# Optimization experiments

Hardware: AMD Instinct MI355X
Metric: run time of the kernel (lower is better)

## Reference

```python
import jax, jax.numpy as jnp
import numpy as np

N = 4096
NHID = 256
K1, K2, K3 = 3072, 2304, 1728


def _layernorm(x, g, b, eps=1e-5):
    m = jnp.mean(x, axis=-1, keepdims=True)
    v = jnp.mean((x - m) ** 2, axis=-1, keepdims=True)
    return (x - m) / jnp.sqrt(v + eps) * g + b


def _gcn(x, A, W, b):
    # PyG GCNConv: add self loops, symmetric norm D^-1/2 (A+I) D^-1/2,
    # messages flow row(source) -> col(target): out[j] = sum_i Anorm[i,j] (xW)[i] + b
    n = A.shape[0]
    A_sl = A + jnp.eye(n, dtype=A.dtype)
    deg = A_sl.sum(0)  # in-degree over col index incl. self loop
    dinv = jnp.where(deg > 0, deg ** -0.5, 0.0)
    An = A_sl * dinv[:, None] * dinv[None, :]
    return An.T @ (x @ W) + b


def _sagpool(x, A, Wp, bp, k):
    score = jnp.tanh(_gcn(x, A, Wp, bp)[:, 0])  # [n]
    vals, perm = jax.lax.top_k(score, k)
    x_new = x[perm] * vals[:, None]
    A_new = A[perm][:, perm]  # induced subgraph of directed edges
    return x_new, A_new


def _readout(x):
    # cat([global_max_pool, global_mean_pool]) for a single graph -> [1, 2*nhid]
    return jnp.concatenate([x.max(0), x.mean(0)])[None, :]


def setup_inputs() -> dict:
    key = jax.random.key(0)
    ks = jax.random.split(key, 10)
    s = 0.05
    return {
        'feature': jax.random.normal(ks[0], (N, 500), jnp.float32),
        'img_info': jax.random.normal(ks[1], (N, 6), jnp.float32),
        'Wp': jax.random.normal(ks[2], (6, 12), jnp.float32) * s,
        'bp': jnp.zeros((12,), jnp.float32),
        'ln_f_g': jnp.ones((500,), jnp.float32),
        'ln_f_b': jnp.zeros((500,), jnp.float32),
        'ln_p_g': jnp.ones((12,), jnp.float32),
        'ln_p_b': jnp.zeros((12,), jnp.float32),
        'W1': jax.random.normal(ks[3], (512, NHID), jnp.float32) * s,
        'b1': jnp.zeros((NHID,), jnp.float32),
        'Wpool1': jax.random.normal(ks[4], (NHID, 1), jnp.float32) * s,
        'bpool1': jnp.zeros((1,), jnp.float32),
        'W2': jax.random.normal(ks[5], (NHID, NHID), jnp.float32) * s,
        'b2': jnp.zeros((NHID,), jnp.float32),
        'Wpool2': jax.random.normal(ks[6], (NHID, 1), jnp.float32) * s,
        'bpool2': jnp.zeros((1,), jnp.float32),
        'W3': jax.random.normal(ks[7], (NHID, NHID), jnp.float32) * s,
        'b3': jnp.zeros((NHID,), jnp.float32),
        'Wpool3': jax.random.normal(ks[8], (NHID, 1), jnp.float32) * s,
        'bpool3': jnp.zeros((1,), jnp.float32),
    }


def reference(feature, img_info, Wp, bp, ln_f_g, ln_f_b, ln_p_g, ln_p_b,
              W1, b1, Wpool1, bpool1, W2, b2, Wpool2, bpool2,
              W3, b3, Wpool3, bpool3):
    # pos embedding + self-attention over nodes
    pos = img_info @ Wp + bp                                  # [N,12]
    att = jax.nn.softmax(pos @ pos.T / jnp.sqrt(12.0), axis=1)  # [N,N]
    pos = att @ pos

    f = _layernorm(feature, ln_f_g, ln_f_b)
    p = _layernorm(pos, ln_p_g, ln_p_b)
    x0 = jnp.concatenate([f, p], axis=1)                      # [N,512]

    # edge construction: upper-triangular directed edges where sqdist < 0.5*max sqdist
    sq = jnp.sum(x0 * x0, axis=1)
    d2 = sq[:, None] - 2.0 * (x0 @ x0.T) + sq[None, :]        # [N,N]
    t = 0.5 * d2.max()
    n = x0.shape[0]
    iu = jnp.triu(jnp.ones((n, n), bool), 1)
    A = jnp.where((d2 < t) & iu, 1.0, 0.0).astype(x0.dtype)

    x = jax.nn.relu(_gcn(x0, A, W1, b1))
    x, A = _sagpool(x, A, Wpool1, bpool1, K1)
    x1 = _readout(x)

    x = jax.nn.relu(_gcn(x, A, W2, b2))
    x, A = _sagpool(x, A, Wpool2, bpool2, K2)
    x2 = _readout(x)

    x = jax.nn.relu(_gcn(x, A, W3, b3))
    x, A = _sagpool(x, A, Wpool3, bpool3, K3)
    x3 = _readout(x)

    return x1 + x2 + x3  # [1, 512]
```

## Files before the change

kernel.cpp:

```cpp
#include <hip/hip_runtime.h>
#include <math.h>

#define NN 4096
#define RB 128

typedef __attribute__((ext_vector_type(8))) short bf16x8;
typedef __attribute__((ext_vector_type(4))) float f32x4;

__device__ __forceinline__ unsigned encf(float f) {
  unsigned u = __float_as_uint(f);
  return (u & 0x80000000u) ? ~u : (u | 0x80000000u);
}
__device__ __forceinline__ float decf(unsigned u) {
  return __uint_as_float((u & 0x80000000u) ? (u ^ 0x80000000u) : ~u);
}
__device__ __forceinline__ unsigned short f2bf(float f) {
  unsigned u = __float_as_uint(f);
  return (unsigned short)((u + 0x7fffu + ((u >> 16) & 1u)) >> 16);
}

__global__ void k_pos(const float* img, const float* Wp, const float* bp, float* pos,
                      unsigned* dmax) {
  if (blockIdx.x == 0 && threadIdx.x == 0) *dmax = 0u;
  int t = blockIdx.x * 256 + threadIdx.x;
  if (t >= NN * 12) return;
  int i = t / 12, d = t % 12;
  float s = bp[d];
#pragma unroll
  for (int k = 0; k < 6; ++k) s += img[i * 6 + k] * Wp[k * 12 + d];
  pos[t] = s;
}

__global__ __launch_bounds__(256) void k_attn3(const float* pos, float* out) {
  __shared__ float sp[12][256];
  int t = threadIdx.x, lane = t & 63, w = t >> 6;
  int ib = blockIdx.x * 8 + w * 2;
  float pi[2][12];
#pragma unroll
  for (int r = 0; r < 2; ++r)
#pragma unroll
    for (int d = 0; d < 12; ++d) pi[r][d] = pos[(ib + r) * 12 + d] * 0.28867513459481287f;
  float sl[2] = {0.f, 0.f};
  float acc[2][12] = {};
  const float4* p4 = (const float4*)pos;
  for (int kt = 0; kt < NN; kt += 256) {
    __syncthreads();
    int j = kt + t;
    float4 a = p4[j * 3 + 0], b = p4[j * 3 + 1], c = p4[j * 3 + 2];
    sp[0][t] = a.x; sp[1][t] = a.y; sp[2][t] = a.z; sp[3][t] = a.w;
    sp[4][t] = b.x; sp[5][t] = b.y; sp[6][t] = b.z; sp[7][t] = b.w;
    sp[8][t] = c.x; sp[9][t] = c.y; sp[10][t] = c.z; sp[11][t] = c.w;
    __syncthreads();
#pragma unroll
    for (int q = 0; q < 4; ++q) {
      int jj = q * 64 + lane;
      float pj[12];
#pragma unroll
      for (int d = 0; d < 12; ++d) pj[d] = sp[d][jj];
#pragma unroll
      for (int r = 0; r < 2; ++r) {
        float s = 0.f;
#pragma unroll
        for (int d = 0; d < 12; ++d) s = fmaf(pi[r][d], pj[d], s);
        float e = __expf(s);
        sl[r] += e;
#pragma unroll
        for (int d = 0; d < 12; ++d) acc[r][d] = fmaf(e, pj[d], acc[r][d]);
      }
    }
  }
#pragma unroll
  for (int r = 0; r < 2; ++r) {
    float s = sl[r];
#pragma unroll
    for (int o = 32; o > 0; o >>= 1) s += __shfl_xor(s, o);
    float ad[12];
#pragma unroll
    for (int d = 0; d < 12; ++d) {
      ad[d] = acc[r][d];
#pragma unroll
      for (int o = 32; o > 0; o >>= 1) ad[d] += __shfl_xor(ad[d], o);
    }
    if (lane == 0) {
      float inv = 1.f / s;
#pragma unroll
      for (int d = 0; d < 12; ++d) out[(ib + r) * 12 + d] = ad[d] * inv;
    }
  }
}

__global__ __launch_bounds__(256) void k_lnx(const float* f, const float* g, const float* b,
                                             const float* p, const float* pg, const float* pb,
                                             float* x0, unsigned short* x0h, float* sqv,
                                             int* degA) {
  __shared__ float row[512];
  __shared__ float wrA[4], wrB[4], wrC[4];
  int i = blockIdx.x, t = threadIdx.x, lane = t & 63, w = t >> 6;
  if (t == 0) degA[i] = 0;
  float v1 = f[i * 500 + t];
  float v2 = (t < 244) ? f[i * 500 + 256 + t] : 0.f;
  float part = v1 + v2;
#pragma unroll
  for (int o = 32; o > 0; o >>= 1) part += __shfl_xor(part, o);
  if (lane == 0) wrA[w] = part;
  __syncthreads();
  float m = (wrA[0] + wrA[1] + wrA[2] + wrA[3]) * (1.f / 500.f);
  float d1 = v1 - m, d2 = v2 - m;
  float pvv = d1 * d1 + ((t < 244) ? d2 * d2 : 0.f);
#pragma unroll
  for (int o = 32; o > 0; o >>= 1) pvv += __shfl_xor(pvv, o);
  if (lane == 0) wrB[w] = pvv;
  __syncthreads();
  float scale = 1.f / sqrtf((wrB[0] + wrB[1] + wrB[2] + wrB[3]) * (1.f / 500.f) + 1e-5f);
  row[t] = d1 * scale * g[t] + b[t];
  if (t < 244) row[256 + t] = d2 * scale * g[256 + t] + b[256 + t];
  if (t >= 244) {
    int tt = t - 244;
    float pv[12], pm = 0.f;
#pragma unroll
    for (int d = 0; d < 12; ++d) { pv[d] = p[i * 12 + d]; pm += pv[d]; }
    pm *= (1.f / 12.f);
    float pvar = 0.f;
#pragma unroll
    for (int d = 0; d < 12; ++d) { float dd = pv[d] - pm; pvar += dd * dd; }
    pvar *= (1.f / 12.f);
    float ps = 1.f / sqrtf(pvar + 1e-5f);
    row[500 + tt] = (pv[tt] - pm) * ps * pg[tt] + pb[tt];
  }
  __syncthreads();
  float a = row[t], c = row[256 + t];
  float sq = a * a + c * c;
#pragma unroll
  for (int o = 32; o > 0; o >>= 1) sq += __shfl_xor(sq, o);
  if (lane == 0) wrC[w] = sq;
  __syncthreads();
  if (t == 0) sqv[i] = wrC[0] + wrC[1] + wrC[2] + wrC[3];
  x0[(size_t)i * 512 + t] = a;
  x0[(size_t)i * 512 + 256 + t] = c;
  x0h[(size_t)i * 512 + t] = f2bf(a);
  x0h[(size_t)i * 512 + 256 + t] = f2bf(c);
}

#define BK 64
template <bool MASK>
__global__ __launch_bounds__(256) void k_d2m(const unsigned short* X, const float* sqv,
                                             unsigned* dmax, float* tileMin,
                                             unsigned char* ATm, int* deg) {
  __shared__ unsigned short As[2][128 * BK];
  __shared__ unsigned short Bs[2][128 * BK];
  __shared__ float wmax[4], wmin[4];
  const int NT = NN / 128;
  int bid0 = blockIdx.x;
  int bid = (bid0 & 7) * 66 + (bid0 >> 3);
  int ti = 0, rem = bid;
  while (rem >= NT - ti) { rem -= NT - ti; ++ti; }
  int tj = ti + rem;
  int t = threadIdx.x, lane = t & 63, w = t >> 6;
  int wr = w >> 1, wc = w & 1;
  const unsigned short* Abase = X + (size_t)ti * 128 * 512;
  const unsigned short* Bbase = X + (size_t)tj * 128 * 512;
  int lr = lane >> 3, lc = lane & 7;

  float thr = 0.f;
  if (MASK) {
    thr = 0.5f * decf(*dmax);
    uint4 z = make_uint4(0u, 0u, 0u, 0u);
    if (ti != tj) {
#pragma unroll
      for (int q0 = 0; q0 < 4; ++q0) {
        int q = t + q0 * 256; int r = q >> 3, c4 = q & 7;
        *(uint4*)(ATm + (size_t)(ti * 128 + r) * NN + tj * 128 + c4 * 16) = z;
      }
    }
    if (tileMin[blockIdx.x] >= thr) {
#pragma unroll
      for (int q0 = 0; q0 < 4; ++q0) {
        int q = t + q0 * 256; int r = q >> 3, c4 = q & 7;
        *(uint4*)(ATm + (size_t)(tj * 128 + r) * NN + ti * 128 + c4 * 16) = z;
      }
      return;
    }
  }

  auto stage = [&](int buf, int k0) {
#pragma unroll
    for (int i = 0; i < 4; ++i) {
      int q = w * 4 + i;
      int r = q * 8 + lr;
      int cs = lc ^ (r & 7);
      __builtin_amdgcn_global_load_lds(
          (const __attribute__((address_space(1))) unsigned int*)(Abase + (size_t)r * 512 + k0 + cs * 8),
          (__attribute__((address_space(3))) unsigned int*)(&As[buf][q * 512]), 16, 0, 0);
      __builtin_amdgcn_global_load_lds(
          (const __attribute__((address_space(1))) unsigned int*)(Bbase + (size_t)r * 512 + k0 + cs * 8),
          (__attribute__((address_space(3))) unsigned int*)(&Bs[buf][q * 512]), 16, 0, 0);
    }
  };

  stage(0, 0);

  f32x4 acc[4][4] = {};
  int rl = lane & 15, kg = lane >> 4;
  for (int step = 0; step < 8; ++step) {
    int cur = step & 1;
    if (step < 7) {
      stage(cur ^ 1, (step + 1) * BK);
      asm volatile("s_waitcnt vmcnt(8)" ::: "memory");
    } else {
      asm volatile("s_waitcnt vmcnt(0)" ::: "memory");
    }
    __builtin_amdgcn_sched_barrier(0);
    __builtin_amdgcn_s_barrier();
    __builtin_amdgcn_s_setprio(1);
#pragma unroll
    for (int ks = 0; ks < 2; ++ks) {
      bf16x8 af[4], bq[4];
#pragma unroll
      for (int f = 0; f < 4; ++f) {
        int rA = wr * 64 + f * 16 + rl;
        af[f] = *(const bf16x8*)(&As[cur][rA * BK + (((ks * 4 + kg) ^ (rA & 7)) << 3)]);
        int rB = wc * 64 + f * 16 + rl;
        bq[f] = *(const bf16x8*)(&Bs[cur][rB * BK + (((ks * 4 + kg) ^ (rB & 7)) << 3)]);
      }
#pragma unroll
      for (int a = 0; a < 4; ++a)
#pragma unroll
        for (int b = 0; b < 4; ++b)
          acc[a][b] = __builtin_amdgcn_mfma_f32_16x16x32_bf16(af[a], bq[b], acc[a][b], 0, 0, 0);
    }
    __builtin_amdgcn_s_setprio(0);
    __builtin_amdgcn_sched_barrier(0);
    __builtin_amdgcn_s_barrier();
  }
  int rbase = ti * 128 + wr * 64 + ((lane >> 4) << 2);
  int cbase = tj * 128 + wc * 64 + (lane & 15);
  if (!MASK) {
    float lm = -1e30f, lmin = 1e30f;
#pragma unroll
    for (int a = 0; a < 4; ++a) {
      float si[4];
#pragma unroll
      for (int r = 0; r < 4; ++r) si[r] = sqv[rbase + a * 16 + r];
#pragma unroll
      for (int b = 0; b < 4; ++b) {
        int gj = cbase + b * 16;
        float sj = sqv[gj];
#pragma unroll
        for (int r = 0; r < 4; ++r) {
          float d2v = si[r] - 2.f * acc[a][b][r] + sj;
          lm = fmaxf(lm, d2v);
          if (rbase + a * 16 + r < gj) lmin = fminf(lmin, d2v);
        }
      }
    }
#pragma unroll
    for (int o = 32; o > 0; o >>= 1) {
      lm = fmaxf(lm, __shfl_xor(lm, o));
      lmin = fminf(lmin, __shfl_xor(lmin, o));
    }
    if (lane == 0) { wmax[w] = lm; wmin[w] = lmin; }
    __syncthreads();
    if (t == 0) {
      atomicMax(dmax, encf(fmaxf(fmaxf(wmax[0], wmax[1]), fmaxf(wmax[2], wmax[3]))));
      tileMin[blockIdx.x] = fminf(fminf(wmin[0], wmin[1]), fminf(wmin[2], wmin[3]));
    }
  } else {
#pragma unroll
    for (int b = 0; b < 4; ++b) {
      int gj = cbase + b * 16;
      float sj = sqv[gj];
      int rowcnt = 0;
#pragma unroll
      for (int a = 0; a < 4; ++a) {
        int gi0 = rbase + a * 16;
        union { unsigned char c[4]; unsigned u; } m4;
#pragma unroll
        for (int r = 0; r < 4; ++r) {
          float d2v = sqv[gi0 + r] - 2.f * acc[a][b][r] + sj;
          unsigned char mv = (d2v < thr && (gi0 + r) < gj) ? 1 : 0;
          m4.c[r] = mv; rowcnt += mv;
        }
        *(unsigned*)(ATm + (size_t)gj * NN + gi0) = m4.u;
      }
      if (rowcnt) atomicAdd(&deg[gj], rowcnt);
    }
  }
}

__global__ __launch_bounds__(256) void k_gemm(const float* A, const float* B, const int* deg,
                                              float* C, int M, int N, int K) {
  __shared__ float Ast[16][34];
  __shared__ float Bs[16][64];
  int t = threadIdx.x, tx = t & 15, ty = t >> 4;
  int nbx = N >> 6;
  int total = gridDim.x;
  int bid0 = blockIdx.x;
  int bid = (bid0 & 7) * (total >> 3) + (bid0 >> 3);
  int m0 = (bid / nbx) * 32, n0 = (bid % nbx) * 64;
  int ar = t >> 3, ac = (t * 2) & 15;
  int br = t >> 4, bc = (t & 15) * 4;
  float2 ra = *(const float2*)(A + (size_t)(m0 + ar) * K + ac);
  float4 rb = *(const float4*)(B + (size_t)br * N + n0 + bc);
  float acc[2][4] = {};
  for (int k0 = 0; k0 < K; k0 += 16) {
    Ast[ac][ar] = ra.x; Ast[ac + 1][ar] = ra.y;
    *(float4*)(&Bs[br][bc]) = rb;
    __syncthreads();
    if (k0 + 16 < K) {
      ra = *(const float2*)(A + (size_t)(m0 + ar) * K + k0 + 16 + ac);
      rb = *(const float4*)(B + (size_t)(k0 + 16 + br) * N + n0 + bc);
    }
#pragma unroll
    for (int kk = 0; kk < 16; ++kk) {
      float2 av = *(const float2*)(&Ast[kk][ty * 2]);
      float4 bv = *(const float4*)(&Bs[kk][tx * 4]);
      acc[0][0] = fmaf(av.x, bv.x, acc[0][0]);
      acc[0][1] = fmaf(av.x, bv.y, acc[0][1]);
      acc[0][2] = fmaf(av.x, bv.z, acc[0][2]);
      acc[0][3] = fmaf(av.x, bv.w, acc[0][3]);
      acc[1][0] = fmaf(av.y, bv.x, acc[1][0]);
      acc[1][1] = fmaf(av.y, bv.y, acc[1][1]);
      acc[1][2] = fmaf(av.y, bv.z, acc[1][2]);
      acc[1][3] = fmaf(av.y, bv.w, acc[1][3]);
    }
    __syncthreads();
  }
#pragma unroll
  for (int a = 0; a < 2; ++a) {
    float dv = 1.f / sqrtf((float)(1 + deg[m0 + ty * 2 + a]));
#pragma unroll
    for (int b2 = 0; b2 < 4; ++b2)
      C[(size_t)(m0 + ty * 2 + a) * N + n0 + tx * 4 + b2] = acc[a][b2] * dv;
  }
}

__global__ __launch_bounds__(256) void k_agg(const float* y, const unsigned char* ATm,
                                             const int* deg, const float* bias,
                                             const float* Wpool, float* out, float* y2, int n) {
  __shared__ unsigned char mrow[256];
  __shared__ int s_any;
  __shared__ float wred[4];
  int j = blockIdx.x, t = threadIdx.x, lane = t & 63, w = t >> 6;
  int dg = deg[j];
  float dj = 1.f / sqrtf((float)(1 + dg));
  float acc = y[(size_t)j * 256 + t];
  if (dg != 0) {
    for (int i0 = 0; i0 < n; i0 += 256) {
      if (t == 0) s_any = 0;
      __syncthreads();
      unsigned char m = ATm[(size_t)j * n + i0 + t];
      mrow[t] = m;
      if (m) s_any = 1;
      __syncthreads();
      if (s_any) {
        for (int u = 0; u < 256; ++u)
          if (mrow[u]) acc += y[(size_t)(i0 + u) * 256 + t];
      }
      __syncthreads();
    }
  }
  float o = fmaxf(dj * acc + bias[t], 0.f);
  out[(size_t)j * 256 + t] = o;
  float rv = o * Wpool[t];
#pragma unroll
  for (int os = 32; os > 0; os >>= 1) rv += __shfl_xor(rv, os);
  if (lane == 0) wred[w] = rv;
  __syncthreads();
  if (t == 0) y2[j] = dj * (wred[0] + wred[1] + wred[2] + wred[3]);
}

__global__ __launch_bounds__(256) void k_scorek(const float* y2, const unsigned char* ATm,
                                                const int* deg, const float* bp,
                                                float* score, int n) {
  int w = threadIdx.x >> 6, lane = threadIdx.x & 63;
  int j = blockIdx.x * 4 + w;
  if (j >= n) return;
  int dg = deg[j];
  float dj = 1.f / sqrtf((float)(1 + dg));
  float s = 0.f;
  if (dg != 0) {
    const uint4* row = (const uint4*)(ATm + (size_t)j * n);
    for (int p = lane; p < n / 16; p += 64) {
      uint4 v = row[p];
      if (v.x | v.y | v.z | v.w) {
        int base = p * 16;
#pragma unroll
        for (int q = 0; q < 4; ++q) {
          unsigned u = (&v.x)[q];
#pragma unroll
          for (int b2 = 0; b2 < 4; ++b2)
            if ((u >> (8 * b2)) & 0xffu) s += y2[base + q * 4 + b2];
        }
      }
    }
    for (int sh = 32; sh > 0; sh >>= 1) s += __shfl_down(s, sh);
  }
  if (lane == 0) score[j] = tanhf(dj * (y2[j] + s) + bp[0]);
}

__global__ __launch_bounds__(1024) void k_topsel(const float* score, int n, int k,
                                                 int* perm, float* vals) {
  __shared__ unsigned keys[4096];
  __shared__ unsigned hist[256];
  __shared__ unsigned s_state[2];
  __shared__ unsigned woff[16];
  int t = threadIdx.x, lane = t & 63, w = t >> 6;
  for (int i = t; i < 4096; i += 1024) keys[i] = (i < n) ? encf(score[i]) : 0u;
  if (t == 0) { s_state[0] = 0u; s_state[1] = (unsigned)k; }
  __syncthreads();

  for (int pass = 0; pass < 4; ++pass) {
    int shift = 24 - pass * 8;
    if (t < 256) hist[t] = 0u;
    __syncthreads();
    unsigned prefix = s_state[0];
    unsigned need = s_state[1];
    unsigned pmask = pass ? (0xFFFFFFFFu << (shift + 8)) : 0u;
    for (int i = t; i < n; i += 1024) {
      unsigned kk = keys[i];
      if ((kk & pmask) == prefix) atomicAdd(&hist[(kk >> shift) & 255u], 1u);
    }
    __syncthreads();
    if (w == 0) {
      unsigned h[4], suf[4];
#pragma unroll
      for (int r = 0; r < 4; ++r) h[r] = hist[lane * 4 + r];
      suf[3] = h[3]; suf[2] = h[2] + suf[3]; suf[1] = h[1] + suf[2]; suf[0] = h[0] + suf[1];
      unsigned lsum = suf[0];
      unsigned s = lsum;
#pragma unroll
      for (int off = 1; off < 64; off <<= 1) {
        unsigned o = __shfl_down(s, off);
        if (lane + off < 64) s += o;
      }
      unsigned Hl = s - lsum;
      int cand = -1; unsigned cumAt = 0, histAt = 0;
#pragma unroll
      for (int r = 0; r < 4; ++r) {
        unsigned c = Hl + suf[r];
        if (c >= need) { cand = lane * 4 + r; cumAt = c; histAt = h[r]; }
      }
      int gmax = cand;
#pragma unroll
      for (int off = 32; off > 0; off >>= 1) {
        int o = __shfl_xor(gmax, off);
        gmax = o > gmax ? o : gmax;
      }
      if (cand == gmax && cand >= 0) {
        s_state[0] = prefix | ((unsigned)cand << shift);
        s_state[1] = need - (cumAt - histAt);
      }
    }
    __syncthreads();
  }
  unsigned cutoff = s_state[0];
  unsigned tcount = s_state[1];
  unsigned G = (unsigned)k - tcount;

  int i0 = t * 4;
  unsigned loc[4], cnt = 0;
#pragma unroll
  for (int r = 0; r < 4; ++r) {
    unsigned kk = keys[i0 + r];
    unsigned g = (kk > cutoff) ? 1u : 0u;
    unsigned e = (kk == cutoff) ? 1u : 0u;
    loc[r] = cnt;
    cnt += (g << 16) | e;
  }
  unsigned inc = cnt;
#pragma unroll
  for (int off = 1; off < 64; off <<= 1) {
    unsigned o = __shfl_up(inc, off);
    if (lane >= off) inc += o;
  }
  if (lane == 63) woff[w] = inc;
  __syncthreads();
  if (t == 0) {
    unsigned run = 0;
    for (int q = 0; q < 16; ++q) { unsigned v = woff[q]; woff[q] = run; run += v; }
  }
  __syncthreads();
  unsigned base = woff[w] + (inc - cnt);
#pragma unroll
  for (int r = 0; r < 4; ++r) {
    unsigned kk = keys[i0 + r];
    unsigned p = base + loc[r];
    if (kk > cutoff) {
      unsigned pos = p >> 16;
      perm[pos] = i0 + r; vals[pos] = decf(kk);
    } else if (kk == cutoff) {
      unsigned pe = p & 0xffffu;
      if (pe < tcount) { perm[G + pe] = i0 + r; vals[G + pe] = decf(kk); }
    }
  }
}

__global__ __launch_bounds__(256) void k_pool(const float* xg, const int* perm, const float* vals,
                                              float* xp, float* pmax, float* psum, int k,
                                              const unsigned char* ATold, const int* degCur,
                                              unsigned char* ATnew, int* degNext, int nold) {
  __shared__ int sperm[4096];
  __shared__ int redi[256];
  int b = blockIdx.x, t = threadIdx.x;
  if (b < RB) {
    float m = -1e30f, s = 0.f;
    for (int r = b; r < k; r += RB) {
      float v = xg[(size_t)perm[r] * 256 + t] * vals[r];
      xp[(size_t)r * 256 + t] = v;
      m = fmaxf(m, v); s += v;
    }
    pmax[b * 256 + t] = m; psum[b * 256 + t] = s;
    return;
  }
  int c = b - RB;
  for (int r = t; r < k; r += 256) sperm[r] = perm[r];
  __syncthreads();
  int src = sperm[c];
  unsigned char* orow = ATnew + (size_t)c * k;
  if (degCur[src] == 0) {
    uint4 z = make_uint4(0u, 0u, 0u, 0u);
    for (int r = t; r < k / 16; r += 256) ((uint4*)orow)[r] = z;
    if (t == 0) degNext[c] = 0;
    return;
  }
  const unsigned char* row = ATold + (size_t)src * nold;
  int cnt = 0;
  for (int r = t; r < k; r += 256) { unsigned char v = row[sperm[r]]; orow[r] = v; cnt += v; }
  redi[t] = cnt; __syncthreads();
  for (int s = 128; s > 0; s >>= 1) { if (t < s) redi[t] += redi[t + s]; __syncthreads(); }
  if (t == 0) degNext[c] = redi[0];
}

__global__ void k_rfin3(const float* pm0, const float* ps0, int k0,
                        const float* pm1, const float* ps1, int k1,
                        const float* pm2, const float* ps2, int k2, float* out) {
  int t = threadIdx.x;
  float m0 = -1e30f, s0 = 0.f, m1 = -1e30f, s1 = 0.f, m2 = -1e30f, s2 = 0.f;
  for (int q = 0; q < RB; ++q) {
    m0 = fmaxf(m0, pm0[q * 256 + t]); s0 += ps0[q * 256 + t];
    m1 = fmaxf(m1, pm1[q * 256 + t]); s1 += ps1[q * 256 + t];
    m2 = fmaxf(m2, pm2[q * 256 + t]); s2 += ps2[q * 256 + t];
  }
  out[t] = m0 + m1 + m2;
  out[256 + t] = s0 / (float)k0 + s1 / (float)k1 + s2 / (float)k2;
}

static void run_layer(hipStream_t stream, const float* x_in, int n, int inC,
                      const float* W, const float* b, const float* Wpool, const float* bpool,
                      int k, const unsigned char* ATcur, unsigned char* ATnext,
                      const int* degCur, int* degNext,
                      float* ybuf, float* xg, float* xp, float* y2,
                      float* score, int* perm, float* vals, float* pmax, float* psum) {
  k_gemm<<<(n / 32) * 4, 256, 0, stream>>>(x_in, W, degCur, ybuf, n, 256, inC);
  k_agg<<<n, 256, 0, stream>>>(ybuf, ATcur, degCur, b, Wpool, xg, y2, n);
  k_scorek<<<n / 4, 256, 0, stream>>>(y2, ATcur, degCur, bpool, score, n);
  k_topsel<<<1, 1024, 0, stream>>>(score, n, k, perm, vals);
  int grid = RB + (ATnext ? k : 0);
  k_pool<<<grid, 256, 0, stream>>>(xg, perm, vals, xp, pmax, psum, k,
                                   ATcur, degCur, ATnext, degNext, n);
}

extern "C" void kernel_launch(void* const* d_in, const int* in_sizes, int n_in,
                              void* d_out, int out_size, void* d_ws, size_t ws_size,
                              hipStream_t stream) {
  const float* feature = (const float*)d_in[0];
  const float* img     = (const float*)d_in[1];
  const float* Wp      = (const float*)d_in[2];
  const float* bp      = (const float*)d_in[3];
  const float* ln_f_g  = (const float*)d_in[4];
  const float* ln_f_b  = (const float*)d_in[5];
  const float* ln_p_g  = (const float*)d_in[6];
  const float* ln_p_b  = (const float*)d_in[7];
  const float* W1 = (const float*)d_in[8];   const float* b1 = (const float*)d_in[9];
  const float* Wpool1 = (const float*)d_in[10]; const float* bpool1 = (const float*)d_in[11];
  const float* W2 = (const float*)d_in[12];  const float* b2 = (const float*)d_in[13];
  const float* Wpool2 = (const float*)d_in[14]; const float* bpool2 = (const float*)d_in[15];
  const float* W3 = (const float*)d_in[16];  const float* b3 = (const float*)d_in[17];
  const float* Wpool3 = (const float*)d_in[18]; const float* bpool3 = (const float*)d_in[19];
  float* out = (float*)d_out;
  (void)in_sizes; (void)n_in; (void)out_size; (void)ws_size;

  char* w = (char*)d_ws;
  size_t off = 0;
  auto alloc = [&](size_t bytes) -> char* {
    off = (off + 255) & ~(size_t)255;
    char* p = w + off;
    off += bytes;
    return p;
  };
  float* pos0 = (float*)alloc((size_t)NN * 12 * 4);
  float* pos1 = (float*)alloc((size_t)NN * 12 * 4);
  float* x0   = (float*)alloc((size_t)NN * 512 * 4);
  unsigned short* x0h = (unsigned short*)alloc((size_t)NN * 512 * 2);
  float* sqv  = (float*)alloc((size_t)NN * 4);
  unsigned* dmax = (unsigned*)alloc(4);
  float* tileMin = (float*)alloc(528 * 4);
  int* degA = (int*)alloc((size_t)NN * 4);
  int* degB = (int*)alloc((size_t)NN * 4);
  float* ybuf = (float*)alloc((size_t)NN * 256 * 4);
  float* xg   = (float*)alloc((size_t)NN * 256 * 4);
  float* xp   = (float*)alloc((size_t)NN * 256 * 4);
  float* y2   = (float*)alloc((size_t)NN * 4);
  float* score= (float*)alloc((size_t)NN * 4);
  int*   perm = (int*)alloc((size_t)NN * 4);
  float* vals = (float*)alloc((size_t)NN * 4);
  float* pmax0 = (float*)alloc(RB * 256 * 4);
  float* psum0 = (float*)alloc(RB * 256 * 4);
  float* pmax1 = (float*)alloc(RB * 256 * 4);
  float* psum1 = (float*)alloc(RB * 256 * 4);
  float* pmax2 = (float*)alloc(RB * 256 * 4);
  float* psum2 = (float*)alloc(RB * 256 * 4);
  unsigned char* ATa = (unsigned char*)alloc((size_t)NN * NN);
  unsigned char* ATb = (unsigned char*)alloc((size_t)3072 * 3072);

  k_pos<<<(NN * 12 + 255) / 256, 256, 0, stream>>>(img, Wp, bp, pos0, dmax);
  k_attn3<<<NN / 8, 256, 0, stream>>>(pos0, pos1);
  k_lnx<<<NN, 256, 0, stream>>>(feature, ln_f_g, ln_f_b, pos1, ln_p_g, ln_p_b,
                                x0, x0h, sqv, degA);

  const int NT = NN / 128, TT = NT * (NT + 1) / 2;
  k_d2m<false><<<TT, 256, 0, stream>>>(x0h, sqv, dmax, tileMin, nullptr, nullptr);
  k_d2m<true><<<TT, 256, 0, stream>>>(x0h, sqv, dmax, tileMin, ATa, degA);

  run_layer(stream, x0, 4096, 512, W1, b1, Wpool1, bpool1, 3072, ATa, ATb, degA, degB,
            ybuf, xg, xp, y2, score, perm, vals, pmax0, psum0);
  run_layer(stream, xp, 3072, 256, W2, b2, Wpool2, bpool2, 2304, ATb, ATa, degB, degA,
            ybuf, xg, xp, y2, score, perm, vals, pmax1, psum1);
  run_layer(stream, xp, 2304, 256, W3, b3, Wpool3, bpool3, 1728, ATa, nullptr, degA, nullptr,
            ybuf, xg, xp, y2, score, perm, vals, pmax2, psum2);
  k_rfin3<<<1, 256, 0, stream>>>(pmax0, psum0, 3072, pmax1, psum1, 2304,
                                 pmax2, psum2, 1728, out);
}
```

Measured before the change: 217.4 us.

## Shrink GEMM tile, move isolated-node scores into agg, skip dead pool writes

The feature GEMM tile drops from 32 to 16 rows, which doubles the block count and makes each thread produce four outputs instead of eight, giving more parallelism for the small row counts. Nodes with zero degree now get their pool score computed in the aggregation kernel, so the score kernel returns early for them. The pool kernel skips zeroing adjacency rows of isolated nodes and only loads the permutation into shared memory when it is needed. The last layer skips writing the pooled features, since nothing reads them. Leaving those adjacency rows unzeroed relies on later kernels never reading rows whose degree is zero.

```diff
diff --git a/kernel.cpp b/kernel.cpp
--- a/kernel.cpp
+++ b/kernel.cpp
@@ -289,54 +289,48 @@
 
 __global__ __launch_bounds__(256) void k_gemm(const float* A, const float* B, const int* deg,
                                               float* C, int M, int N, int K) {
-  __shared__ float Ast[16][34];
+  __shared__ float Ast[16][17];
   __shared__ float Bs[16][64];
   int t = threadIdx.x, tx = t & 15, ty = t >> 4;
   int nbx = N >> 6;
   int total = gridDim.x;
   int bid0 = blockIdx.x;
   int bid = (bid0 & 7) * (total >> 3) + (bid0 >> 3);
-  int m0 = (bid / nbx) * 32, n0 = (bid % nbx) * 64;
-  int ar = t >> 3, ac = (t * 2) & 15;
+  int m0 = (bid / nbx) * 16, n0 = (bid % nbx) * 64;
+  int ar = t >> 4, ac = t & 15;
   int br = t >> 4, bc = (t & 15) * 4;
-  float2 ra = *(const float2*)(A + (size_t)(m0 + ar) * K + ac);
+  float ra = A[(size_t)(m0 + ar) * K + ac];
   float4 rb = *(const float4*)(B + (size_t)br * N + n0 + bc);
-  float acc[2][4] = {};
+  float acc[4] = {};
   for (int k0 = 0; k0 < K; k0 += 16) {
-    Ast[ac][ar] = ra.x; Ast[ac + 1][ar] = ra.y;
+    Ast[ac][ar] = ra;
     *(float4*)(&Bs[br][bc]) = rb;
     __syncthreads();
     if (k0 + 16 < K) {
-      ra = *(const float2*)(A + (size_t)(m0 + ar) * K + k0 + 16 + ac);
+      ra = A[(size_t)(m0 + ar) * K + k0 + 16 + ac];
       rb = *(const float4*)(B + (size_t)(k0 + 16 + br) * N + n0 + bc);
     }
 #pragma unroll
     for (int kk = 0; kk < 16; ++kk) {
-      float2 av = *(const float2*)(&Ast[kk][ty * 2]);
+      float av = Ast[kk][ty];
       float4 bv = *(const float4*)(&Bs[kk][tx * 4]);
-      acc[0][0] = fmaf(av.x, bv.x, acc[0][0]);
-      acc[0][1] = fmaf(av.x, bv.y, acc[0][1]);
-      acc[0][2] = fmaf(av.x, bv.z, acc[0][2]);
-      acc[0][3] = fmaf(av.x, bv.w, acc[0][3]);
-      acc[1][0] = fmaf(av.y, bv.x, acc[1][0]);
-      acc[1][1] = fmaf(av.y, bv.y, acc[1][1]);
-      acc[1][2] = fmaf(av.y, bv.z, acc[1][2]);
-      acc[1][3] = fmaf(av.y, bv.w, acc[1][3]);
-    }
-    __syncthreads();
-  }
-#pragma unroll
-  for (int a = 0; a < 2; ++a) {
-    float dv = 1.f / sqrtf((float)(1 + deg[m0 + ty * 2 + a]));
-#pragma unroll
-    for (int b2 = 0; b2 < 4; ++b2)
-      C[(size_t)(m0 + ty * 2 + a) * N + n0 + tx * 4 + b2] = acc[a][b2] * dv;
-  }
+      acc[0] = fmaf(av, bv.x, acc[0]);
+      acc[1] = fmaf(av, bv.y, acc[1]);
+      acc[2] = fmaf(av, bv.z, acc[2]);
+      acc[3] = fmaf(av, bv.w, acc[3]);
+    }
+    __syncthreads();
+  }
+  float dv = 1.f / sqrtf((float)(1 + deg[m0 + ty]));
+#pragma unroll
+  for (int b2 = 0; b2 < 4; ++b2)
+    C[(size_t)(m0 + ty) * N + n0 + tx * 4 + b2] = acc[b2] * dv;
 }
 
 __global__ __launch_bounds__(256) void k_agg(const float* y, const unsigned char* ATm,
                                              const int* deg, const float* bias,
-                                             const float* Wpool, float* out, float* y2, int n) {
+                                             const float* Wpool, const float* bp,
+                                             float* out, float* y2, float* score, int n) {
   __shared__ unsigned char mrow[256];
   __shared__ int s_any;
   __shared__ float wred[4];
@@ -366,7 +360,11 @@
   for (int os = 32; os > 0; os >>= 1) rv += __shfl_xor(rv, os);
   if (lane == 0) wred[w] = rv;
   __syncthreads();
-  if (t == 0) y2[j] = dj * (wred[0] + wred[1] + wred[2] + wred[3]);
+  if (t == 0) {
+    float yy = dj * (wred[0] + wred[1] + wred[2] + wred[3]);
+    y2[j] = yy;
+    if (dg == 0) score[j] = tanhf(dj * yy + bp[0]);
+  }
 }
 
 __global__ __launch_bounds__(256) void k_scorek(const float* y2, const unsigned char* ATm,
@@ -376,25 +374,24 @@
   int j = blockIdx.x * 4 + w;
   if (j >= n) return;
   int dg = deg[j];
+  if (dg == 0) return;
   float dj = 1.f / sqrtf((float)(1 + dg));
   float s = 0.f;
-  if (dg != 0) {
-    const uint4* row = (const uint4*)(ATm + (size_t)j * n);
-    for (int p = lane; p < n / 16; p += 64) {
-      uint4 v = row[p];
-      if (v.x | v.y | v.z | v.w) {
-        int base = p * 16;
-#pragma unroll
-        for (int q = 0; q < 4; ++q) {
-          unsigned u = (&v.x)[q];
-#pragma unroll
-          for (int b2 = 0; b2 < 4; ++b2)
-            if ((u >> (8 * b2)) & 0xffu) s += y2[base + q * 4 + b2];
-        }
-      }
-    }
-    for (int sh = 32; sh > 0; sh >>= 1) s += __shfl_down(s, sh);
-  }
+  const uint4* row = (const uint4*)(ATm + (size_t)j * n);
+  for (int p = lane; p < n / 16; p += 64) {
+    uint4 v = row[p];
+    if (v.x | v.y | v.z | v.w) {
+      int base = p * 16;
+#pragma unroll
+      for (int q = 0; q < 4; ++q) {
+        unsigned u = (&v.x)[q];
+#pragma unroll
+        for (int b2 = 0; b2 < 4; ++b2)
+          if ((u >> (8 * b2)) & 0xffu) s += y2[base + q * 4 + b2];
+      }
+    }
+  }
+  for (int sh = 32; sh > 0; sh >>= 1) s += __shfl_down(s, sh);
   if (lane == 0) score[j] = tanhf(dj * (y2[j] + s) + bp[0]);
 }
 
@@ -506,23 +503,21 @@
     float m = -1e30f, s = 0.f;
     for (int r = b; r < k; r += RB) {
       float v = xg[(size_t)perm[r] * 256 + t] * vals[r];
-      xp[(size_t)r * 256 + t] = v;
+      if (xp) xp[(size_t)r * 256 + t] = v;
       m = fmaxf(m, v); s += v;
     }
     pmax[b * 256 + t] = m; psum[b * 256 + t] = s;
     return;
   }
   int c = b - RB;
-  for (int r = t; r < k; r += 256) sperm[r] = perm[r];
-  __syncthreads();
-  int src = sperm[c];
-  unsigned char* orow = ATnew + (size_t)c * k;
+  int src = perm[c];
   if (degCur[src] == 0) {
-    uint4 z = make_uint4(0u, 0u, 0u, 0u);
-    for (int r = t; r < k / 16; r += 256) ((uint4*)orow)[r] = z;
     if (t == 0) degNext[c] = 0;
     return;
   }
+  for (int r = t; r < k; r += 256) sperm[r] = perm[r];
+  __syncthreads();
+  unsigned char* orow = ATnew + (size_t)c * k;
   const unsigned char* row = ATold + (size_t)src * nold;
   int cnt = 0;
   for (int r = t; r < k; r += 256) { unsigned char v = row[sperm[r]]; orow[r] = v; cnt += v; }
@@ -551,12 +546,12 @@
                       const int* degCur, int* degNext,
                       float* ybuf, float* xg, float* xp, float* y2,
                       float* score, int* perm, float* vals, float* pmax, float* psum) {
-  k_gemm<<<(n / 32) * 4, 256, 0, stream>>>(x_in, W, degCur, ybuf, n, 256, inC);
-  k_agg<<<n, 256, 0, stream>>>(ybuf, ATcur, degCur, b, Wpool, xg, y2, n);
+  k_gemm<<<(n / 16) * 4, 256, 0, stream>>>(x_in, W, degCur, ybuf, n, 256, inC);
+  k_agg<<<n, 256, 0, stream>>>(ybuf, ATcur, degCur, b, Wpool, bpool, xg, y2, score, n);
   k_scorek<<<n / 4, 256, 0, stream>>>(y2, ATcur, degCur, bpool, score, n);
   k_topsel<<<1, 1024, 0, stream>>>(score, n, k, perm, vals);
   int grid = RB + (ATnext ? k : 0);
-  k_pool<<<grid, 256, 0, stream>>>(xg, perm, vals, xp, pmax, psum, k,
+  k_pool<<<grid, 256, 0, stream>>>(xg, perm, vals, ATnext ? xp : nullptr, pmax, psum, k,
                                    ATcur, degCur, ATnext, degNext, n);
 }
 
```

Result: no change. 220.4 us (+1.4%).
